# Kernel tuning notes

Hardware: AMD Instinct MI355X
Metric: run time of the kernel (lower is better)

The kernel has to match this reference:

```python
import jax, jax.numpy as jnp
import numpy as np

B, L, P, C, K, NL, DF = 32, 512, 96, 512, 8, 2, 512
CK = C // K
EPS = 1e-5


def setup_inputs() -> dict:
    key = jax.random.key(0)
    ks = jax.random.split(key, 6)
    s = lambda k, shape, fan: jax.random.normal(k, shape, jnp.float32) / np.float32(np.sqrt(fan))
    return dict(
        x=jax.random.normal(ks[0], (B, L, C), jnp.float32),
        cluster_ids=jnp.arange(C, dtype=jnp.int32),
        rev_w=jnp.ones((C,), jnp.float32),
        rev_b=jnp.zeros((C,), jnp.float32),
        Wt=s(ks[1], (K, NL, L, L), L),
        bt=jnp.zeros((K, NL, L), jnp.float32),
        ln1_g=jnp.ones((K, NL, CK), jnp.float32),
        ln1_b=jnp.zeros((K, NL, CK), jnp.float32),
        Wf1=s(ks[2], (K, NL, CK, DF), CK),
        bf1=jnp.zeros((K, NL, DF), jnp.float32),
        Wf2=s(ks[3], (K, NL, DF, CK), DF),
        bf2=jnp.zeros((K, NL, CK), jnp.float32),
        ln2_g=jnp.ones((K, NL, CK), jnp.float32),
        ln2_b=jnp.zeros((K, NL, CK), jnp.float32),
        Wout=s(ks[4], (K, L, P), L),
        bout=jnp.zeros((K, P), jnp.float32),
    )


def _ln(y, g, b):
    # y: [K,B,L,Ck]; g,b: [K,Ck] -- per-cluster layernorm over channel dim
    m = y.mean(-1, keepdims=True)
    v = y.var(-1, keepdims=True)
    return (y - m) * jax.lax.rsqrt(v + EPS) * g[:, None, None, :] + b[:, None, None, :]


def reference(x, cluster_ids, rev_w, rev_b, Wt, bt, ln1_g, ln1_b,
              Wf1, bf1, Wf2, bf2, ln2_g, ln2_b, Wout, bout):
    # RevIN norm (instance norm over time axis)
    mean = x.mean(axis=1, keepdims=True)
    std = jnp.sqrt(x.var(axis=1, keepdims=True) + EPS)
    xn = (x - mean) / std * rev_w + rev_b

    Kc = Wt.shape[0]
    Ck = cluster_ids.shape[0] // Kc
    assign = cluster_ids % Kc                 # hard cluster assignment per channel
    perm = jnp.argsort(assign)                # stable -> groups channels by cluster
    idx = perm.reshape(Kc, Ck)                # [K, Ck] channel ids per cluster

    # gather: [B,L,K,Ck] -> [K,B,L,Ck]
    xg = jnp.transpose(xn[:, :, idx], (2, 0, 1, 3))

    for l in range(Wt.shape[1]):
        # time mixing: Linear over seq dim, per cluster
        y = _ln(xg, ln1_g[:, l], ln1_b[:, l])
        y = jax.nn.relu(jnp.einsum('kblc,klm->kbmc', y, Wt[:, l]) + bt[:, l][:, None, :, None])
        xg = xg + y
        # feature mixing: Linear over channel dim, per cluster
        y = _ln(xg, ln2_g[:, l], ln2_b[:, l])
        y = jax.nn.relu(jnp.einsum('kblc,kcf->kblf', y, Wf1[:, l]) + bf1[:, l][:, None, None, :])
        y = jnp.einsum('kblf,kfc->kblc', y, Wf2[:, l]) + bf2[:, l][:, None, None, :]
        xg = xg + y

    # temporal projection seq_len -> pred_len: [K,B,P,Ck]
    out = jnp.einsum('kblc,klp->kbpc', xg, Wout) + bout[:, None, :, None]

    # scatter back to full channel layout
    flat = jnp.transpose(out, (1, 2, 0, 3)).reshape(x.shape[0], Wout.shape[-1], -1)
    full = jnp.zeros_like(flat).at[:, :, perm].set(flat)

    # RevIN denorm
    return (full - rev_b) / rev_w * std + mean
```

## Files before the change

### kernel.cpp

```cpp
#include <hip/hip_runtime.h>

typedef unsigned short u16;
typedef unsigned int   u32;
typedef __attribute__((ext_vector_type(8))) __bf16 bf16x8;
typedef __attribute__((ext_vector_type(4))) float  f32x4;

#define DEV __device__ __forceinline__

namespace {

constexpr int B_  = 32;
constexpr int L_  = 512;
constexpr int P_  = 96;
constexpr int C_  = 512;
constexpr int K_  = 8;
constexpr int NL_ = 2;
constexpr int DF_ = 512;
constexpr int CK_ = 64;
constexpr float EPS_ = 1e-5f;

DEV float bf2f(u16 u){ union { u32 i; float f; } t; t.i = ((u32)u) << 16; return t.f; }
DEV u16 f2bf(float f){ union { float f; u32 i; } t; t.f = f;
  u32 r = t.i + 0x7fffu + ((t.i >> 16) & 1u); return (u16)(r >> 16); }
DEV u16 f2bfn(float f){ __bf16 h = (__bf16)f; u16 u; __builtin_memcpy(&u, &h, 2); return u; }
DEV float LD(const void* p, size_t i, int bf){
  return bf ? bf2f(((const u16*)p)[i]) : ((const float*)p)[i];
}

__global__ __launch_bounds__(256) void k_probe(const u32* __restrict__ x, int* __restrict__ flag){
  int cnt = 0;
  for (int i = threadIdx.x; i < 4096; i += 256){
    u32 w = x[i];
    u32 e = (w >> 7) & 0xFFu;
    cnt += (e >= 0x70u && e <= 0x8Fu) ? 1 : 0;
  }
#pragma unroll
  for (int o = 32; o > 0; o >>= 1) cnt += __shfl_xor(cnt, o);
  __shared__ int s[4];
  if ((threadIdx.x & 63) == 0) s[threadIdx.x >> 6] = cnt;
  __syncthreads();
  if (threadIdx.x == 0) flag[0] = (s[0] + s[1] + s[2] + s[3] > 2048) ? 1 : 0;
}

__global__ __launch_bounds__(512) void k_sort(const int* __restrict__ cid, int* __restrict__ idx){
  __shared__ int bkt[C_];
  __shared__ int cnt[K_];
  __shared__ int off[K_];
  int c = threadIdx.x;
  int v = cid[c] % K_; if (v < 0) v += K_;
  bkt[c] = v;
  __syncthreads();
  if (c < K_){ int n = 0; for (int i = 0; i < C_; i++) n += (bkt[i] == c); cnt[c] = n; }
  __syncthreads();
  if (c == 0){ int s = 0; for (int k = 0; k < K_; k++){ off[k] = s; s += cnt[k]; } }
  __syncthreads();
  int r = 0;
  for (int i = 0; i < c; i++) r += (bkt[i] == bkt[c]);
  idx[off[bkt[c]] + r] = c;
}

__global__ __launch_bounds__(256) void k_trans(const void* __restrict__ in, u16* __restrict__ out,
                                               int R, int Cn, const int* __restrict__ flagp){
  __shared__ u16 t[32][36];
  int bf = *flagp;
  int z = blockIdx.z;
  int r0 = blockIdx.y * 32, c0 = blockIdx.x * 32;
  size_t base = (size_t)z * R * Cn;
  int tid = threadIdx.x;
  int i = tid >> 3, j4 = (tid & 7) * 4;
  size_t off = base + (size_t)(r0 + i) * Cn + c0 + j4;
  if (bf){
    ushort4 v = *reinterpret_cast<const ushort4*>((const u16*)in + off);
    t[i][j4 + 0] = v.x; t[i][j4 + 1] = v.y; t[i][j4 + 2] = v.z; t[i][j4 + 3] = v.w;
  } else {
    float4 v = *reinterpret_cast<const float4*>((const float*)in + off);
    t[i][j4 + 0] = f2bf(v.x); t[i][j4 + 1] = f2bf(v.y); t[i][j4 + 2] = f2bf(v.z); t[i][j4 + 3] = f2bf(v.w);
  }
  __syncthreads();
  ushort4 w;
  w.x = t[j4 + 0][i]; w.y = t[j4 + 1][i]; w.z = t[j4 + 2][i]; w.w = t[j4 + 3][i];
  *reinterpret_cast<ushort4*>(out + base + (size_t)(c0 + i) * R + r0 + j4) = w;
}

__global__ __launch_bounds__(512) void k_stats1(const void* __restrict__ x,
                                                float* __restrict__ psum, float* __restrict__ psq,
                                                const int* __restrict__ flagp){
  int bf = *flagp;
  int ls = blockIdx.x, b = blockIdx.y, c = threadIdx.x;
  size_t base = ((size_t)b * L_ + (size_t)ls * 32) * C_ + c;
  float s = 0.f, sq = 0.f;
#pragma unroll 8
  for (int l = 0; l < 32; l++){
    float v = LD(x, base + (size_t)l * C_, bf);
    s += v; sq += v * v;
  }
  int o = (b * 16 + ls) * C_ + c;
  psum[o] = s; psq[o] = sq;
}

__global__ __launch_bounds__(512) void k_stats2(const float* __restrict__ psum, const float* __restrict__ psq,
                                                const void* __restrict__ revw, const void* __restrict__ revb,
                                                float* __restrict__ meanw, float* __restrict__ stdw,
                                                float* __restrict__ scalew, float* __restrict__ biasw,
                                                const int* __restrict__ flagp){
  int bf = *flagp;
  int b = blockIdx.x, c = threadIdx.x;
  float s = 0.f, sq = 0.f;
#pragma unroll
  for (int i = 0; i < 16; i++){
    s  += psum[(b * 16 + i) * C_ + c];
    sq += psq [(b * 16 + i) * C_ + c];
  }
  float m = s * (1.f / L_);
  float var = sq * (1.f / L_) - m * m;
  float sd = sqrtf(var + EPS_);
  meanw[b * C_ + c] = m;
  stdw [b * C_ + c] = sd;
  float sc = LD(revw, c, bf) / sd;
  scalew[b * C_ + c] = sc;
  biasw [b * C_ + c] = LD(revb, c, bf) - m * sc;
}

__global__ __launch_bounds__(256) void k_gather(const void* __restrict__ x, const int* __restrict__ idx,
                                                const float* __restrict__ scalew, const float* __restrict__ biasw,
                                                float* __restrict__ xg, const int* __restrict__ flagp){
  __shared__ float row[576];
  int bf = *flagp;
  int lt = blockIdx.x, b = blockIdx.y;
  int tid = threadIdx.x;
  int oc0 = tid, oc1 = tid + 256;
  int c0 = idx[oc0], c1 = idx[oc1];
  float sc0 = scalew[b * C_ + c0], bs0 = biasw[b * C_ + c0];
  float sc1 = scalew[b * C_ + c1], bs1 = biasw[b * C_ + c1];
  int p0 = c0 + (c0 >> 3), p1 = c1 + (c1 >> 3);
  int k0 = oc0 >> 6, j0 = oc0 & 63;
  int k1 = oc1 >> 6, j1 = oc1 & 63;

  for (int r = 0; r < 16; r++){
    int l = lt * 16 + r;
    size_t base = ((size_t)b * L_ + l) * C_;
    if (bf){
      int i4 = tid * 2;
      ushort2 v = *reinterpret_cast<const ushort2*>((const u16*)x + base + i4);
      int a0 = i4, a1 = i4 + 1;
      row[a0 + (a0 >> 3)] = bf2f(v.x);
      row[a1 + (a1 >> 3)] = bf2f(v.y);
    } else {
      int i2 = tid * 2;
      float2 v = *reinterpret_cast<const float2*>((const float*)x + base + i2);
      int a0 = i2, a1 = i2 + 1;
      row[a0 + (a0 >> 3)] = v.x;
      row[a1 + (a1 >> 3)] = v.y;
    }
    __syncthreads();
    float o0 = row[p0] * sc0 + bs0;
    float o1 = row[p1] * sc1 + bs1;
    xg[(((size_t)k0 * B_ + b) * L_ + l) * CK_ + j0] = o0;
    xg[(((size_t)k1 * B_ + b) * L_ + l) * CK_ + j1] = o1;
    __syncthreads();
  }
}

__global__ __launch_bounds__(256) void k_lnt(const float* __restrict__ src, u16* __restrict__ dst,
                                             const void* __restrict__ g, const void* __restrict__ bb,
                                             int layer, int use_ln, const int* __restrict__ flagp){
  __shared__ float tile[64][65];
  int bf = *flagp;
  int z = blockIdx.x;
  int kb = z >> 3, lt = z & 7;
  int k = kb >> 5;
  const float* s = src + (size_t)kb * L_ * CK_ + (size_t)lt * 64 * CK_;
  int tid = threadIdx.x, lane = tid & 63, w = tid >> 6;
  float gj = 1.f, bj = 0.f;
  if (use_ln){
    gj = LD(g,  (size_t)(k * NL_ + layer) * CK_ + lane, bf);
    bj = LD(bb, (size_t)(k * NL_ + layer) * CK_ + lane, bf);
  }
  for (int i = 0; i < 16; i++){
    int row = w * 16 + i;
    float v = s[(size_t)row * CK_ + lane];
    float sum = v, sq = v * v;
#pragma unroll
    for (int o = 32; o > 0; o >>= 1){ sum += __shfl_xor(sum, o); sq += __shfl_xor(sq, o); }
    float nv = v;
    if (use_ln){
      float m = sum * (1.f / 64.f);
      float var = sq * (1.f / 64.f) - m * m;
      nv = (v - m) * rsqrtf(var + EPS_) * gj + bj;
    }
    tile[row][lane] = nv;
  }
  __syncthreads();
  int c = tid >> 2, seg = tid & 3;
  union { u16 s[8]; uint4 q; } u0, u1;
#pragma unroll
  for (int e = 0; e < 8; e++) u0.s[e] = f2bf(tile[seg * 16 + e][c]);
#pragma unroll
  for (int e = 0; e < 8; e++) u1.s[e] = f2bf(tile[seg * 16 + 8 + e][c]);
  u16* d = dst + (size_t)kb * CK_ * L_ + (size_t)c * L_ + lt * 64 + seg * 16;
  *reinterpret_cast<uint4*>(d)     = u0.q;
  *reinterpret_cast<uint4*>(d + 8) = u1.q;
}

__global__ __launch_bounds__(256, 4) void k_time(const u16* __restrict__ WtT, const u16* __restrict__ xpt,
                                                 float* __restrict__ xg, u16* __restrict__ xp,
                                                 const void* __restrict__ bt,
                                                 const void* __restrict__ ln2g, const void* __restrict__ ln2b,
                                                 int layer, const int* __restrict__ flagp){
  __shared__ u16 a_lds[128 * 40];
  __shared__ u16 b_lds[64 * 40];
  int bf = *flagp;
  int bid = blockIdx.x;
  int k = bid & 7, rr = bid >> 3;
  int b = rr & 31, mb = rr >> 5;
  int m0 = mb * 128;
  const int klb = k * NL_ + layer;
  const u16* A  = WtT + ((size_t)klb * L_ + m0) * L_;
  const u16* Bm = xpt + (size_t)(k * B_ + b) * CK_ * L_;
  int tid = threadIdx.x, lane = tid & 63, w = tid >> 6, grp = lane >> 4, ln = lane & 15;

  int sa0 = tid, sa1 = tid + 256;
  int ra0 = sa0 >> 2, qa0 = (sa0 & 3) * 8;
  int ra1 = sa1 >> 2, qa1 = (sa1 & 3) * 8;
  int rb0 = tid >> 2, qb0 = (tid & 3) * 8;

  f32x4 acc[2][4];
#pragma unroll
  for (int i = 0; i < 2; i++)
#pragma unroll
    for (int j = 0; j < 4; j++) acc[i][j] = (f32x4){0.f, 0.f, 0.f, 0.f};

  uint4 va0 = *reinterpret_cast<const uint4*>(A + (size_t)ra0 * L_ + qa0);
  uint4 va1 = *reinterpret_cast<const uint4*>(A + (size_t)ra1 * L_ + qa1);
  uint4 vb0 = *reinterpret_cast<const uint4*>(Bm + (size_t)rb0 * L_ + qb0);

  for (int kk = 0; kk < 16; kk++){
    *reinterpret_cast<uint4*>(&a_lds[ra0 * 40 + qa0]) = va0;
    *reinterpret_cast<uint4*>(&a_lds[ra1 * 40 + qa1]) = va1;
    *reinterpret_cast<uint4*>(&b_lds[rb0 * 40 + qb0]) = vb0;
    uint4 na0, na1, nb0;
    if (kk < 15){
      int c0 = (kk + 1) * 32;
      na0 = *reinterpret_cast<const uint4*>(A + (size_t)ra0 * L_ + c0 + qa0);
      na1 = *reinterpret_cast<const uint4*>(A + (size_t)ra1 * L_ + c0 + qa1);
      nb0 = *reinterpret_cast<const uint4*>(Bm + (size_t)rb0 * L_ + c0 + qb0);
    }
    __syncthreads();
    bf16x8 af[2], bfr[4];
#pragma unroll
    for (int mt = 0; mt < 2; mt++)
      af[mt] = *reinterpret_cast<bf16x8*>(&a_lds[(w * 32 + mt * 16 + ln) * 40 + grp * 8]);
#pragma unroll
    for (int ct = 0; ct < 4; ct++)
      bfr[ct] = *reinterpret_cast<bf16x8*>(&b_lds[(ct * 16 + ln) * 40 + grp * 8]);
#pragma unroll
    for (int mt = 0; mt < 2; mt++)
#pragma unroll
      for (int ct = 0; ct < 4; ct++)
        acc[mt][ct] = __builtin_amdgcn_mfma_f32_16x16x32_bf16(af[mt], bfr[ct], acc[mt][ct], 0, 0, 0);
    __syncthreads();
    va0 = na0; va1 = na1; vb0 = nb0;
  }

  float g2[4], b2[4];
#pragma unroll
  for (int ct = 0; ct < 4; ct++){
    int cc = ct * 16 + ln;
    g2[ct] = LD(ln2g, (size_t)klb * CK_ + cc, bf);
    b2[ct] = LD(ln2b, (size_t)klb * CK_ + cc, bf);
  }
  float* xgp = xg + (size_t)(k * B_ + b) * L_ * CK_;
  u16*  xpw = xp + (size_t)(k * B_ + b) * L_ * CK_;
#pragma unroll
  for (int mt = 0; mt < 2; mt++){
#pragma unroll
    for (int r = 0; r < 4; r++){
      int m = m0 + w * 32 + mt * 16 + grp * 4 + r;
      float bias = LD(bt, (size_t)klb * L_ + m, bf);
      float xn[4];
      float s = 0.f, sq = 0.f;
#pragma unroll
      for (int ct = 0; ct < 4; ct++){
        int cc = ct * 16 + ln;
        float y = fmaxf(acc[mt][ct][r] + bias, 0.f);
        float v = xgp[(size_t)m * CK_ + cc] + y;
        xgp[(size_t)m * CK_ + cc] = v;
        xn[ct] = v; s += v; sq += v * v;
      }
#pragma unroll
      for (int o = 1; o < 16; o <<= 1){ s += __shfl_xor(s, o); sq += __shfl_xor(sq, o); }
      float mean = s * (1.f / 64.f);
      float var = sq * (1.f / 64.f) - mean * mean;
      float rstd = rsqrtf(var + EPS_);
#pragma unroll
      for (int ct = 0; ct < 4; ct++){
        int cc = ct * 16 + ln;
        xpw[(size_t)m * CK_ + cc] = f2bfn((xn[ct] - mean) * rstd * g2[ct] + b2[ct]);
      }
    }
  }
}

__global__ __launch_bounds__(512, 4) void k_feat(const u16* __restrict__ xp, const u16* __restrict__ w1t,
                                                 const u16* __restrict__ w2t, float* __restrict__ xg,
                                                 const void* __restrict__ bf1, const void* __restrict__ bf2,
                                                 int layer, const int* __restrict__ flagp){
  __shared__ u16 sm[256 * 72];
  __shared__ u16 wl[2][64 * 72];
  int bf = *flagp;
  int lt = blockIdx.x, b = blockIdx.y, k = blockIdx.z;
  int kb = k * B_ + b;
  const u16* xpp = xp + ((size_t)kb * L_ + lt * 256) * CK_;
  const u16* w1p = w1t + (size_t)(k * NL_ + layer) * DF_ * CK_;
  const u16* w2p = w2t + (size_t)(k * NL_ + layer) * CK_ * DF_;
  int tid = threadIdx.x, lane = tid & 63, w = tid >> 6, grp = lane >> 4, ln = lane & 15;
  int wr0 = tid >> 3, wq0 = (tid & 7) * 8;

#pragma unroll
  for (int s = tid; s < 2048; s += 512){
    int row = s >> 3, q = s & 7;
    *reinterpret_cast<uint4*>(&sm[row * 72 + q * 8]) =
      *reinterpret_cast<const uint4*>(xpp + (size_t)row * CK_ + q * 8);
  }
  uint4 g1a = *reinterpret_cast<const uint4*>(w1p + (size_t)wr0 * CK_ + wq0);
  uint4 g2a = *reinterpret_cast<const uint4*>(w2p + (size_t)wr0 * DF_ + wq0);
  __syncthreads();
  bf16x8 af[2][2];
#pragma unroll
  for (int mt = 0; mt < 2; mt++)
#pragma unroll
    for (int ks = 0; ks < 2; ks++)
      af[mt][ks] = *reinterpret_cast<bf16x8*>(&sm[(w * 32 + mt * 16 + ln) * 72 + ks * 32 + grp * 8]);
  __syncthreads();

  f32x4 acc2[2][4];
#pragma unroll
  for (int i = 0; i < 2; i++)
#pragma unroll
    for (int j = 0; j < 4; j++) acc2[i][j] = (f32x4){0.f, 0.f, 0.f, 0.f};

  const int klb = (k * NL_ + layer);
#pragma unroll
  for (int ft = 0; ft < 8; ft++){
    *reinterpret_cast<uint4*>(&wl[0][wr0 * 72 + wq0]) = g1a;
    *reinterpret_cast<uint4*>(&wl[1][wr0 * 72 + wq0]) = g2a;
    if (ft < 7){
      g1a = *reinterpret_cast<const uint4*>(w1p + (size_t)((ft + 1) * 64 + wr0) * CK_ + wq0);
      g2a = *reinterpret_cast<const uint4*>(w2p + (size_t)wr0 * DF_ + (ft + 1) * 64 + wq0);
    }
    __syncthreads();

    f32x4 acc1[2][4];
#pragma unroll
    for (int i = 0; i < 2; i++)
#pragma unroll
      for (int j = 0; j < 4; j++) acc1[i][j] = (f32x4){0.f, 0.f, 0.f, 0.f};
#pragma unroll
    for (int ks = 0; ks < 2; ks++)
#pragma unroll
      for (int n = 0; n < 4; n++){
        bf16x8 bb = *reinterpret_cast<bf16x8*>(&wl[0][(n * 16 + ln) * 72 + ks * 32 + grp * 8]);
#pragma unroll
        for (int mt = 0; mt < 2; mt++)
          acc1[mt][n] = __builtin_amdgcn_mfma_f32_16x16x32_bf16(af[mt][ks], bb, acc1[mt][n], 0, 0, 0);
      }
#pragma unroll
    for (int n = 0; n < 4; n++){
      float bias = LD(bf1, (size_t)klb * DF_ + ft * 64 + n * 16 + ln, bf);
#pragma unroll
      for (int mt = 0; mt < 2; mt++)
#pragma unroll
        for (int r = 0; r < 4; r++){
          float v = fmaxf(acc1[mt][n][r] + bias, 0.f);
          sm[(w * 32 + mt * 16 + grp * 4 + r) * 72 + n * 16 + ln] = f2bfn(v);
        }
    }
#pragma unroll
    for (int ks = 0; ks < 2; ks++){
      bf16x8 hh[2];
#pragma unroll
      for (int mt = 0; mt < 2; mt++)
        hh[mt] = *reinterpret_cast<bf16x8*>(&sm[(w * 32 + mt * 16 + ln) * 72 + ks * 32 + grp * 8]);
#pragma unroll
      for (int n = 0; n < 4; n++){
        bf16x8 bb = *reinterpret_cast<bf16x8*>(&wl[1][(n * 16 + ln) * 72 + ks * 32 + grp * 8]);
#pragma unroll
        for (int mt = 0; mt < 2; mt++)
          acc2[mt][n] = __builtin_amdgcn_mfma_f32_16x16x32_bf16(hh[mt], bb, acc2[mt][n], 0, 0, 0);
      }
    }
    __syncthreads();
  }

  float* xgp = xg + ((size_t)kb * L_ + lt * 256) * CK_;
#pragma unroll
  for (int n = 0; n < 4; n++){
    int cc = n * 16 + ln;
    float b2 = LD(bf2, (size_t)klb * CK_ + cc, bf);
#pragma unroll
    for (int mt = 0; mt < 2; mt++)
#pragma unroll
      for (int r = 0; r < 4; r++){
        int rl = w * 32 + mt * 16 + grp * 4 + r;
        xgp[(size_t)rl * CK_ + cc] += acc2[mt][n][r] + b2;
      }
  }
}

__global__ __launch_bounds__(384) void k_out(const u16* __restrict__ WoT, const u16* __restrict__ xgt,
                                             const int* __restrict__ idx, const void* __restrict__ bout,
                                             const void* __restrict__ revw, const void* __restrict__ revb,
                                             const float* __restrict__ meanw, const float* __restrict__ stdw,
                                             void* __restrict__ out, const int* __restrict__ flagp){
  __shared__ u16 a_lds[96 * 40];
  __shared__ u16 b_lds[64 * 40];
  int bf = *flagp;
  int b = blockIdx.x, k = blockIdx.y;
  int kb = k * B_ + b;
  const u16* A  = WoT + (size_t)k * P_ * L_;
  const u16* Bm = xgt + (size_t)kb * CK_ * L_;
  int tid = threadIdx.x, lane = tid & 63, w = tid >> 6, grp = lane >> 4, ln = lane & 15;
  f32x4 acc[4];
#pragma unroll
  for (int j = 0; j < 4; j++) acc[j] = (f32x4){0.f, 0.f, 0.f, 0.f};

  for (int kk = 0; kk < 16; kk++){
    {
      int row = tid >> 2, q = tid & 3;
      *reinterpret_cast<uint4*>(&a_lds[row * 40 + q * 8]) =
        *reinterpret_cast<const uint4*>(A + (size_t)row * L_ + kk * 32 + q * 8);
    }
    if (tid < 256){
      int row = tid >> 2, q = tid & 3;
      *reinterpret_cast<uint4*>(&b_lds[row * 40 + q * 8]) =
        *reinterpret_cast<const uint4*>(Bm + (size_t)row * L_ + kk * 32 + q * 8);
    }
    __syncthreads();
    bf16x8 af = *reinterpret_cast<bf16x8*>(&a_lds[(w * 16 + ln) * 40 + grp * 8]);
#pragma unroll
    for (int n = 0; n < 4; n++){
      bf16x8 bfr = *reinterpret_cast<bf16x8*>(&b_lds[(n * 16 + ln) * 40 + grp * 8]);
      acc[n] = __builtin_amdgcn_mfma_f32_16x16x32_bf16(af, bfr, acc[n], 0, 0, 0);
    }
    __syncthreads();
  }
#pragma unroll
  for (int n = 0; n < 4; n++){
    int j = n * 16 + ln;
    int c = idx[k * CK_ + j];
    float rw = LD(revw, c, bf), rb = LD(revb, c, bf);
    float sd = stdw[b * C_ + c], mn = meanw[b * C_ + c];
#pragma unroll
    for (int r = 0; r < 4; r++){
      int p = w * 16 + grp * 4 + r;
      float y = acc[n][r] + LD(bout, (size_t)k * P_ + p, bf);
      float val = (y - rb) / rw * sd + mn;
      size_t oi = ((size_t)b * P_ + p) * C_ + c;
      if (bf) ((u16*)out)[oi] = f2bf(val);
      else    ((float*)out)[oi] = val;
    }
  }
}

}

extern "C" void kernel_launch(void* const* d_in, const int* in_sizes, int n_in,
                              void* d_out, int out_size, void* d_ws, size_t ws_size,
                              hipStream_t stream){
  const void* x    = d_in[0];
  const int*  cid  = (const int*)d_in[1];
  const void* revw = d_in[2];
  const void* revb = d_in[3];
  const void* Wt   = d_in[4];
  const void* bt   = d_in[5];
  const void* ln1g = d_in[6];
  const void* ln1b = d_in[7];
  const void* Wf1  = d_in[8];
  const void* bf1  = d_in[9];
  const void* Wf2  = d_in[10];
  const void* bf2  = d_in[11];
  const void* ln2g = d_in[12];
  const void* ln2b = d_in[13];
  const void* Wout = d_in[14];
  const void* bout = d_in[15];
  char* ws = (char*)d_ws;

  int*   flag   = (int*)  (ws + 0);
  int*   idxp   = (int*)  (ws + 64);
  float* meanw  = (float*)(ws + 4096);
  float* stdw   = (float*)(ws + 69632);
  float* scalew = (float*)(ws + 135168);
  float* biasw  = (float*)(ws + 200704);
  float* psum   = (float*)(ws + 266240);
  float* psq    = (float*)(ws + 1314816);
  float* xg     = (float*)(ws + 2363392);
  u16*   xs     = (u16*)  (ws + 35917824);
  u16*   WtT    = (u16*)  (ws + 52695040);
  u16*   Wf1T   = (u16*)  (ws + 61083648);
  u16*   Wf2T   = (u16*)  (ws + 62132224);
  u16*   WoT    = (u16*)  (ws + 63180800);
  u16*   xp2    = (u16*)  (ws + 63967232);

  k_probe<<<1, 256, 0, stream>>>((const u32*)x, flag);
  k_sort<<<1, 512, 0, stream>>>(cid, idxp);
  k_trans<<<dim3(16, 16, 16), 256, 0, stream>>>(Wt,   WtT,  512, 512, flag);
  k_trans<<<dim3(16,  2, 16), 256, 0, stream>>>(Wf1,  Wf1T,  64, 512, flag);
  k_trans<<<dim3( 2, 16, 16), 256, 0, stream>>>(Wf2,  Wf2T, 512,  64, flag);
  k_trans<<<dim3( 3, 16,  8), 256, 0, stream>>>(Wout, WoT,  512,  96, flag);
  k_stats1<<<dim3(16, 32), 512, 0, stream>>>(x, psum, psq, flag);
  k_stats2<<<32, 512, 0, stream>>>(psum, psq, revw, revb, meanw, stdw, scalew, biasw, flag);
  k_gather<<<dim3(32, 32), 256, 0, stream>>>(x, idxp, scalew, biasw, xg, flag);

  for (int layer = 0; layer < NL_; layer++){
    k_lnt<<<2048, 256, 0, stream>>>(xg, xs, ln1g, ln1b, layer, 1, flag);
    k_time<<<1024, 256, 0, stream>>>(WtT, xs, xg, xp2, bt, ln2g, ln2b, layer, flag);
    k_feat<<<dim3(2, 32, 8), 512, 0, stream>>>(xp2, Wf1T, Wf2T, xg, bf1, bf2, layer, flag);
  }

  k_lnt<<<2048, 256, 0, stream>>>(xg, xs, nullptr, nullptr, 0, 0, flag);
  k_out<<<dim3(32, 8), 384, 0, stream>>>(WoT, xs, idxp, bout, revw, revb, meanw, stdw, d_out, flag);
}
```

Baseline: 264.3 us.

## Fuse next-layer LayerNorm and transpose into feature-mixing epilogue

The feature-mixing kernel's epilogue now applies the next layer's time-mixing LayerNorm, or a plain transposed bf16 copy on the last layer. It stages the result transposed in shared memory and writes the channel-major bf16 buffer the next time-mixing or output kernel consumes. This removes two standalone k_lnt launches and their full re-read of the fp32 residual stream. The cost is extra shuffles, an extra barrier and reuse of the input tile's shared-memory buffer in k_feat.

```diff
diff --git a/kernel.cpp b/kernel.cpp
--- a/kernel.cpp
+++ b/kernel.cpp
@@ -304,7 +304,9 @@
 __global__ __launch_bounds__(512, 4) void k_feat(const u16* __restrict__ xp, const u16* __restrict__ w1t,
                                                  const u16* __restrict__ w2t, float* __restrict__ xg,
                                                  const void* __restrict__ bf1, const void* __restrict__ bf2,
-                                                 int layer, const int* __restrict__ flagp){
+                                                 const void* __restrict__ ln1g, const void* __restrict__ ln1b,
+                                                 u16* __restrict__ xsout, int layer,
+                                                 const int* __restrict__ flagp){
   __shared__ u16 sm[256 * 72];
   __shared__ u16 wl[2][64 * 72];
   int bf = *flagp;
@@ -392,18 +394,56 @@
     __syncthreads();
   }
 
-  float* xgp = xg + ((size_t)kb * L_ + lt * 256) * CK_;
+  const int next = layer + 1;
+  const int use_ln = (next < NL_);
+  float g1v[4], b1v[4], b2v[4];
 #pragma unroll
   for (int n = 0; n < 4; n++){
     int cc = n * 16 + ln;
-    float b2 = LD(bf2, (size_t)klb * CK_ + cc, bf);
-#pragma unroll
-    for (int mt = 0; mt < 2; mt++)
-#pragma unroll
-      for (int r = 0; r < 4; r++){
-        int rl = w * 32 + mt * 16 + grp * 4 + r;
-        xgp[(size_t)rl * CK_ + cc] += acc2[mt][n][r] + b2;
-      }
+    b2v[n] = LD(bf2, (size_t)klb * CK_ + cc, bf);
+    if (use_ln){
+      g1v[n] = LD(ln1g, (size_t)(k * NL_ + next) * CK_ + cc, bf);
+      b1v[n] = LD(ln1b, (size_t)(k * NL_ + next) * CK_ + cc, bf);
+    } else { g1v[n] = 1.f; b1v[n] = 0.f; }
+  }
+  float* xgp = xg + ((size_t)kb * L_ + lt * 256) * CK_;
+#pragma unroll
+  for (int mt = 0; mt < 2; mt++){
+#pragma unroll
+    for (int r = 0; r < 4; r++){
+      int rl = w * 32 + mt * 16 + grp * 4 + r;
+      float v[4];
+      float s = 0.f, sq = 0.f;
+#pragma unroll
+      for (int n = 0; n < 4; n++){
+        int cc = n * 16 + ln;
+        float t = xgp[(size_t)rl * CK_ + cc] + acc2[mt][n][r] + b2v[n];
+        xgp[(size_t)rl * CK_ + cc] = t;
+        v[n] = t; s += t; sq += t * t;
+      }
+      float mean = 0.f, rstd = 1.f;
+      if (use_ln){
+#pragma unroll
+        for (int o = 1; o < 16; o <<= 1){ s += __shfl_xor(s, o); sq += __shfl_xor(sq, o); }
+        mean = s * (1.f / 64.f);
+        float var = sq * (1.f / 64.f) - mean * mean;
+        rstd = rsqrtf(var + EPS_);
+      }
+#pragma unroll
+      for (int n = 0; n < 4; n++){
+        int cc = n * 16 + ln;
+        sm[cc * 264 + rl] = f2bfn((v[n] - mean) * rstd * g1v[n] + b1v[n]);
+      }
+    }
+  }
+  __syncthreads();
+  u16* xsw = xsout + (size_t)kb * CK_ * L_ + lt * 256;
+#pragma unroll
+  for (int i = 0; i < 4; i++){
+    int s = tid + i * 512;
+    int c = s >> 5, off = (s & 31) * 8;
+    *reinterpret_cast<uint4*>(xsw + (size_t)c * L_ + off) =
+      *reinterpret_cast<uint4*>(&sm[c * 264 + off]);
   }
 }
 
@@ -511,12 +551,12 @@
   k_stats2<<<32, 512, 0, stream>>>(psum, psq, revw, revb, meanw, stdw, scalew, biasw, flag);
   k_gather<<<dim3(32, 32), 256, 0, stream>>>(x, idxp, scalew, biasw, xg, flag);
 
+  k_lnt<<<2048, 256, 0, stream>>>(xg, xs, ln1g, ln1b, 0, 1, flag);
   for (int layer = 0; layer < NL_; layer++){
-    k_lnt<<<2048, 256, 0, stream>>>(xg, xs, ln1g, ln1b, layer, 1, flag);
     k_time<<<1024, 256, 0, stream>>>(WtT, xs, xg, xp2, bt, ln2g, ln2b, layer, flag);
-    k_feat<<<dim3(2, 32, 8), 512, 0, stream>>>(xp2, Wf1T, Wf2T, xg, bf1, bf2, layer, flag);
-  }
-
-  k_lnt<<<2048, 256, 0, stream>>>(xg, xs, nullptr, nullptr, 0, 0, flag);
+    k_feat<<<dim3(2, 32, 8), 512, 0, stream>>>(xp2, Wf1T, Wf2T, xg, bf1, bf2,
+                                               ln1g, ln1b, xs, layer, flag);
+  }
+
   k_out<<<dim3(32, 8), 384, 0, stream>>>(WoT, xs, idxp, bout, revw, revb, meanw, stdw, d_out, flag);
 }
```

Measured after the change: 231.8 us. 12.3% less time.
